# Kernel optimization log

Hardware: AMD Instinct MI355X
Metric: run time of the kernel (lower is better)

## Reference

```python
import jax, jax.numpy as jnp
import numpy as np

CHAMFER_WEIGHT = 1.0
REG_WEIGHT = 0.1


def setup_inputs() -> dict:
    key = jax.random.key(0)
    k1, k2, k3 = jax.random.split(key, 3)
    B, N, M, K = 16, 4096, 4096, 64
    return {
        "predicted_points": jax.random.normal(k1, (B, N, 3), dtype=jnp.float32),
        "ground_truth_points": jax.random.normal(k2, (B, M, 3), dtype=jnp.float32),
        "trans_feat": jax.random.normal(k3, (B, K, K), dtype=jnp.float32),
    }


def _chamfer(pred, target):
    # Euclidean (non-squared) pairwise distances, matching torch.cdist.
    # Gram trick avoids materializing [B,N,M,3].
    p2 = jnp.sum(pred * pred, axis=-1)          # [B,N]
    t2 = jnp.sum(target * target, axis=-1)      # [B,M]
    cross = jnp.einsum("bnd,bmd->bnm", pred, target)  # [B,N,M]
    d2 = p2[:, :, None] + t2[:, None, :] - 2.0 * cross
    dist = jnp.sqrt(jnp.maximum(d2, 0.0))       # [B,N,M]
    min1 = jnp.min(dist, axis=2)                # [B,N] pred -> nearest target
    min2 = jnp.min(dist, axis=1)                # [B,M] target -> nearest pred
    return jnp.mean(jnp.mean(min1, axis=1) + jnp.mean(min2, axis=1))


def _feature_transform_reg(trans):
    K = trans.shape[1]
    I = jnp.eye(K, dtype=trans.dtype)
    gram = jnp.einsum("bik,bjk->bij", trans, trans)  # trans @ trans^T
    # Frobenius norm per batch element, then mean over batch
    return jnp.mean(jnp.sqrt(jnp.sum((gram - I) ** 2, axis=(1, 2))))


def reference(predicted_points, ground_truth_points, trans_feat):
    chamfer = _chamfer(predicted_points, ground_truth_points)
    reg = _feature_transform_reg(trans_feat)
    return CHAMFER_WEIGHT * chamfer + REG_WEIGHT * reg
```

## Files before the change

### kernel.cpp

```cpp
#include <hip/hip_runtime.h>
#include <math.h>

#define BB 16
#define NN 4096
#define MM 4096
#define CHUNK_COLS 2048
#define NCHUNK (MM / CHUNK_COLS)

typedef __attribute__((ext_vector_type(8))) short bf16x8;
typedef __attribute__((ext_vector_type(16))) float f32x16;

static __device__ inline unsigned short f2bf(float f) {
    unsigned int u = __float_as_uint(f);
    return (unsigned short)((u + 0x7FFFu + ((u >> 16) & 1u)) >> 16);
}
static __device__ inline bf16x8 bzero() {
    bf16x8 z;
    #pragma unroll
    for (int i = 0; i < 8; ++i) z[i] = 0;
    return z;
}
static __device__ inline f32x16 fzero() {
    f32x16 z;
    #pragma unroll
    for (int i = 0; i < 16; ++i) z[i] = 0.f;
    return z;
}

__global__ __launch_bounds__(256, 4) void chamfer_kernel(
    const float* __restrict__ pred, const float* __restrict__ gt,
    float* __restrict__ out)
{
    __shared__ __align__(16) float smem[8832];
    __shared__ float ssum[4];

    const int tid  = threadIdx.x;
    const int lane = tid & 63;
    const int w    = tid >> 6;
    const int li   = lane & 31;
    const int hi   = lane >> 5;
    const int b    = blockIdx.y;
    const int dir  = blockIdx.z;
    const float* rows = dir ? gt : pred;
    const float* cols = dir ? pred : gt;
    const float* rb = rows + (size_t)b * NN * 3;
    const float* cb = cols + (size_t)b * MM * 3;

    const int r0 = blockIdx.x * 256 + w * 64;
    bf16x8 A0 = bzero(), A1 = bzero();
    if (lane < 32) {
        #pragma unroll
        for (int f = 0; f < 2; ++f) {
            const float* rp = rb + (size_t)(r0 + f * 32 + li) * 3;
            const float px = rp[0], py = rp[1], pz = rp[2];
            const float p2 = px * px + py * py + pz * pz;
            bf16x8 fr = bzero();
            fr[0] = (short)f2bf(-2.f * px);
            fr[1] = (short)f2bf(-2.f * py);
            fr[2] = (short)f2bf(-2.f * pz);
            fr[3] = (short)f2bf(p2);
            fr[4] = (short)0x3F80;
            if (f == 0) A0 = fr; else A1 = fr;
        }
    }

    float mv0[16], mv1[16];
    #pragma unroll
    for (int r = 0; r < 16; ++r) { mv0[r] = 3.4e38f; mv1[r] = 3.4e38f; }

    uint4* sB = (uint4*)smem;
    const bf16x8* sBf = (const bf16x8*)smem;

    for (int ch = 0; ch < NCHUNK; ++ch) {
        __syncthreads();
        #pragma unroll
        for (int i = 0; i < CHUNK_COLS / 256; ++i) {
            const int c = i * 256 + tid;
            const float* tp = cb + (size_t)(ch * CHUNK_COLS + c) * 3;
            const float tx = tp[0], ty = tp[1], tz = tp[2];
            const float t2 = tx * tx + ty * ty + tz * tz;
            uint4 pk;
            pk.x = (unsigned)f2bf(tx) | ((unsigned)f2bf(ty) << 16);
            pk.y = (unsigned)f2bf(tz) | (0x3F80u << 16);
            pk.z = (unsigned)f2bf(t2);
            pk.w = 0u;
            sB[c] = pk;
        }
        __syncthreads();

        #pragma unroll 2
        for (int jt = 0; jt < CHUNK_COLS / 64; ++jt) {
            bf16x8 b1 = bzero(), b2 = bzero();
            if (lane < 32) {
                b1 = sBf[jt * 64 + li];
                b2 = sBf[jt * 64 + 32 + li];
            }
            f32x16 a11 = __builtin_amdgcn_mfma_f32_32x32x16_bf16(A0, b1, fzero(), 0, 0, 0);
            f32x16 a12 = __builtin_amdgcn_mfma_f32_32x32x16_bf16(A0, b2, fzero(), 0, 0, 0);
            #pragma unroll
            for (int r = 0; r < 16; ++r)
                mv0[r] = fminf(fminf(a11[r], a12[r]), mv0[r]);
            f32x16 a21 = __builtin_amdgcn_mfma_f32_32x32x16_bf16(A1, b1, fzero(), 0, 0, 0);
            f32x16 a22 = __builtin_amdgcn_mfma_f32_32x32x16_bf16(A1, b2, fzero(), 0, 0, 0);
            #pragma unroll
            for (int r = 0; r < 16; ++r)
                mv1[r] = fminf(fminf(a21[r], a22[r]), mv1[r]);
        }
    }

    __syncthreads();
    {
        float* wb = smem + w * 2208 + li * 68;
        #pragma unroll
        for (int q = 0; q < 4; ++q) {
            const int rl = q * 8 + hi * 4;
            *(float4*)&wb[rl]      = make_float4(mv0[4*q], mv0[4*q+1], mv0[4*q+2], mv0[4*q+3]);
            *(float4*)&wb[rl + 32] = make_float4(mv1[4*q], mv1[4*q+1], mv1[4*q+2], mv1[4*q+3]);
        }
    }
    __syncthreads();

    const float* rbm = smem + (tid >> 6) * 2208 + (tid & 63);
    float m = 3.4e38f;
    #pragma unroll
    for (int c = 0; c < 32; ++c) m = fminf(m, rbm[c * 68]);
    float d = sqrtf(fmaxf(m, 0.0f));

    #pragma unroll
    for (int off = 32; off > 0; off >>= 1)
        d += __shfl_down(d, off, 64);
    if (lane == 0) ssum[w] = d;
    __syncthreads();
    if (tid == 0) {
        const float s = ssum[0] + ssum[1] + ssum[2] + ssum[3];
        atomicAdd(out, s * (1.0f / ((float)BB * (float)NN)));
    }
}

__global__ __launch_bounds__(64) void reg_kernel(
    const float* __restrict__ trans, float* __restrict__ out)
{
    const int b = blockIdx.x;
    const int lane = threadIdx.x;
    const int hi = lane >> 5, li = lane & 31;
    const float* T = trans + (size_t)b * 64 * 64;

    bf16x8 frag[2][4];
    #pragma unroll
    for (int h = 0; h < 2; ++h) {
        #pragma unroll
        for (int s = 0; s < 4; ++s) {
            const float* rp = T + (size_t)(h * 32 + li) * 64 + s * 16 + hi * 8;
            const float4 u0 = *(const float4*)rp;
            const float4 u1 = *(const float4*)(rp + 4);
            bf16x8 fr;
            fr[0] = (short)f2bf(u0.x); fr[1] = (short)f2bf(u0.y);
            fr[2] = (short)f2bf(u0.z); fr[3] = (short)f2bf(u0.w);
            fr[4] = (short)f2bf(u1.x); fr[5] = (short)f2bf(u1.y);
            fr[6] = (short)f2bf(u1.z); fr[7] = (short)f2bf(u1.w);
            frag[h][s] = fr;
        }
    }

    float fsum = 0.f;
    #pragma unroll
    for (int fi = 0; fi < 2; ++fi) {
        #pragma unroll
        for (int fj = 0; fj < 2; ++fj) {
            f32x16 a = fzero();
            #pragma unroll
            for (int s = 0; s < 4; ++s)
                a = __builtin_amdgcn_mfma_f32_32x32x16_bf16(frag[fi][s], frag[fj][s], a, 0, 0, 0);
            #pragma unroll
            for (int r = 0; r < 16; ++r) {
                const int row = fi * 32 + (r & 3) + 8 * (r >> 2) + 4 * hi;
                const int col = fj * 32 + li;
                const float d = a[r] - ((row == col) ? 1.0f : 0.0f);
                fsum = fmaf(d, d, fsum);
            }
        }
    }

    #pragma unroll
    for (int off = 32; off > 0; off >>= 1)
        fsum += __shfl_down(fsum, off, 64);
    if (lane == 0)
        atomicAdd(out, (0.1f / (float)BB) * sqrtf(fsum));
}

extern "C" void kernel_launch(void* const* d_in, const int* in_sizes, int n_in,
                              void* d_out, int out_size, void* d_ws, size_t ws_size,
                              hipStream_t stream)
{
    const float* pred  = (const float*)d_in[0];
    const float* gt    = (const float*)d_in[1];
    const float* trans = (const float*)d_in[2];
    float* out = (float*)d_out;

    hipMemsetAsync(out, 0, sizeof(float), stream);
    reg_kernel<<<dim3(BB), dim3(64), 0, stream>>>(trans, out);
    chamfer_kernel<<<dim3(NN / 256, BB, 2), dim3(256), 0, stream>>>(pred, gt, out);
}
```

Baseline: 32.80 us.

## Split column range across blocks with atomicMin merge and a separate finish kernel

Each chamfer block now covers only half of the column points, which doubles the grid so more blocks run per CU. Partial row minima are merged through an order-preserving unsigned atomicMin into a workspace buffer, and a new finish kernel takes the sqrt and the mean. The inner loop also prefetches the next LDS B fragments into registers, and the chunk loop with its repeated barriers is gone. The cost is a workspace memset, global atomics and one extra kernel launch.

Result: slower. 39.03 us (+19.0%).

```diff
diff --git a/kernel.cpp b/kernel.cpp
--- a/kernel.cpp
+++ b/kernel.cpp
@@ -4,8 +4,9 @@
 #define BB 16
 #define NN 4096
 #define MM 4096
-#define CHUNK_COLS 2048
-#define NCHUNK (MM / CHUNK_COLS)
+#define NSLICE 2
+#define SLICE_COLS (MM / NSLICE)
+#define NROWS_TOTAL (2 * BB * NN)
 
 typedef __attribute__((ext_vector_type(8))) short bf16x8;
 typedef __attribute__((ext_vector_type(16))) float f32x16;
@@ -27,26 +28,27 @@
     return z;
 }
 
-__global__ __launch_bounds__(256, 4) void chamfer_kernel(
+__global__ __launch_bounds__(256, 4) void chamfer_min_kernel(
     const float* __restrict__ pred, const float* __restrict__ gt,
-    float* __restrict__ out)
+    unsigned int* __restrict__ wsmin)
 {
     __shared__ __align__(16) float smem[8832];
-    __shared__ float ssum[4];
 
     const int tid  = threadIdx.x;
     const int lane = tid & 63;
     const int w    = tid >> 6;
     const int li   = lane & 31;
     const int hi   = lane >> 5;
+    const int tile   = blockIdx.x >> 1;
+    const int mslice = blockIdx.x & (NSLICE - 1);
     const int b    = blockIdx.y;
     const int dir  = blockIdx.z;
     const float* rows = dir ? gt : pred;
     const float* cols = dir ? pred : gt;
     const float* rb = rows + (size_t)b * NN * 3;
-    const float* cb = cols + (size_t)b * MM * 3;
-
-    const int r0 = blockIdx.x * 256 + w * 64;
+    const float* cb = cols + ((size_t)b * MM + (size_t)mslice * SLICE_COLS) * 3;
+
+    const int r0 = tile * 256 + w * 64;
     bf16x8 A0 = bzero(), A1 = bzero();
     if (lane < 32) {
         #pragma unroll
@@ -64,48 +66,45 @@
         }
     }
 
+    uint4* sB = (uint4*)smem;
+    #pragma unroll
+    for (int i = 0; i < SLICE_COLS / 256; ++i) {
+        const int c = i * 256 + tid;
+        const float* tp = cb + (size_t)c * 3;
+        const float tx = tp[0], ty = tp[1], tz = tp[2];
+        const float t2 = tx * tx + ty * ty + tz * tz;
+        uint4 pk;
+        pk.x = (unsigned)f2bf(tx) | ((unsigned)f2bf(ty) << 16);
+        pk.y = (unsigned)f2bf(tz) | (0x3F80u << 16);
+        pk.z = (unsigned)f2bf(t2);
+        pk.w = 0u;
+        sB[c] = pk;
+    }
+    __syncthreads();
+
     float mv0[16], mv1[16];
     #pragma unroll
     for (int r = 0; r < 16; ++r) { mv0[r] = 3.4e38f; mv1[r] = 3.4e38f; }
 
-    uint4* sB = (uint4*)smem;
     const bf16x8* sBf = (const bf16x8*)smem;
 
-    for (int ch = 0; ch < NCHUNK; ++ch) {
-        __syncthreads();
-        #pragma unroll
-        for (int i = 0; i < CHUNK_COLS / 256; ++i) {
-            const int c = i * 256 + tid;
-            const float* tp = cb + (size_t)(ch * CHUNK_COLS + c) * 3;
-            const float tx = tp[0], ty = tp[1], tz = tp[2];
-            const float t2 = tx * tx + ty * ty + tz * tz;
-            uint4 pk;
-            pk.x = (unsigned)f2bf(tx) | ((unsigned)f2bf(ty) << 16);
-            pk.y = (unsigned)f2bf(tz) | (0x3F80u << 16);
-            pk.z = (unsigned)f2bf(t2);
-            pk.w = 0u;
-            sB[c] = pk;
-        }
-        __syncthreads();
-
-        #pragma unroll 2
-        for (int jt = 0; jt < CHUNK_COLS / 64; ++jt) {
-            bf16x8 b1 = bzero(), b2 = bzero();
-            if (lane < 32) {
-                b1 = sBf[jt * 64 + li];
-                b2 = sBf[jt * 64 + 32 + li];
-            }
-            f32x16 a11 = __builtin_amdgcn_mfma_f32_32x32x16_bf16(A0, b1, fzero(), 0, 0, 0);
-            f32x16 a12 = __builtin_amdgcn_mfma_f32_32x32x16_bf16(A0, b2, fzero(), 0, 0, 0);
-            #pragma unroll
-            for (int r = 0; r < 16; ++r)
-                mv0[r] = fminf(fminf(a11[r], a12[r]), mv0[r]);
-            f32x16 a21 = __builtin_amdgcn_mfma_f32_32x32x16_bf16(A1, b1, fzero(), 0, 0, 0);
-            f32x16 a22 = __builtin_amdgcn_mfma_f32_32x32x16_bf16(A1, b2, fzero(), 0, 0, 0);
-            #pragma unroll
-            for (int r = 0; r < 16; ++r)
-                mv1[r] = fminf(fminf(a21[r], a22[r]), mv1[r]);
-        }
+    bf16x8 b1 = sBf[li], b2 = sBf[32 + li];
+    for (int jt = 0; jt < SLICE_COLS / 64; ++jt) {
+        const bf16x8 c1 = b1, c2 = b2;
+        if (jt + 1 < SLICE_COLS / 64) {
+            b1 = sBf[(jt + 1) * 64 + li];
+            b2 = sBf[(jt + 1) * 64 + 32 + li];
+        }
+        f32x16 a11 = __builtin_amdgcn_mfma_f32_32x32x16_bf16(A0, c1, fzero(), 0, 0, 0);
+        f32x16 a12 = __builtin_amdgcn_mfma_f32_32x32x16_bf16(A0, c2, fzero(), 0, 0, 0);
+        #pragma unroll
+        for (int r = 0; r < 16; ++r)
+            mv0[r] = fminf(fminf(a11[r], a12[r]), mv0[r]);
+        f32x16 a21 = __builtin_amdgcn_mfma_f32_32x32x16_bf16(A1, c1, fzero(), 0, 0, 0);
+        f32x16 a22 = __builtin_amdgcn_mfma_f32_32x32x16_bf16(A1, c2, fzero(), 0, 0, 0);
+        #pragma unroll
+        for (int r = 0; r < 16; ++r)
+            mv1[r] = fminf(fminf(a21[r], a22[r]), mv1[r]);
     }
 
     __syncthreads();
@@ -120,16 +119,31 @@
     }
     __syncthreads();
 
-    const float* rbm = smem + (tid >> 6) * 2208 + (tid & 63);
+    const float* rbm = smem + w * 2208 + lane;
     float m = 3.4e38f;
     #pragma unroll
     for (int c = 0; c < 32; ++c) m = fminf(m, rbm[c * 68]);
-    float d = sqrtf(fmaxf(m, 0.0f));
+
+    unsigned int u = __float_as_uint(m);
+    u = (u & 0x80000000u) ? ~u : (u | 0x80000000u);
+    const int rowg = (dir * BB + b) * NN + r0 + lane;
+    atomicMin(&wsmin[rowg], u);
+}
+
+__global__ __launch_bounds__(256) void chamfer_finish_kernel(
+    const unsigned int* __restrict__ wsmin, float* __restrict__ out)
+{
+    const int g = blockIdx.x * 256 + threadIdx.x;
+    unsigned int u = wsmin[g];
+    const unsigned int bts = (u & 0x80000000u) ? (u & 0x7fffffffu) : ~u;
+    float d = sqrtf(fmaxf(__uint_as_float(bts), 0.0f));
 
     #pragma unroll
     for (int off = 32; off > 0; off >>= 1)
         d += __shfl_down(d, off, 64);
-    if (lane == 0) ssum[w] = d;
+    __shared__ float ssum[4];
+    const int tid = threadIdx.x;
+    if ((tid & 63) == 0) ssum[tid >> 6] = d;
     __syncthreads();
     if (tid == 0) {
         const float s = ssum[0] + ssum[1] + ssum[2] + ssum[3];
@@ -196,8 +210,13 @@
     const float* gt    = (const float*)d_in[1];
     const float* trans = (const float*)d_in[2];
     float* out = (float*)d_out;
+    unsigned int* wsmin = (unsigned int*)d_ws;
 
     hipMemsetAsync(out, 0, sizeof(float), stream);
+    hipMemsetAsync(wsmin, 0xFF, (size_t)NROWS_TOTAL * sizeof(unsigned int), stream);
+
     reg_kernel<<<dim3(BB), dim3(64), 0, stream>>>(trans, out);
-    chamfer_kernel<<<dim3(NN / 256, BB, 2), dim3(256), 0, stream>>>(pred, gt, out);
-}
+    chamfer_min_kernel<<<dim3((NN / 256) * NSLICE, BB, 2), dim3(256), 0, stream>>>(
+        pred, gt, wsmin);
+    chamfer_finish_kernel<<<dim3(NROWS_TOTAL / 256), dim3(256), 0, stream>>>(wsmin, out);
+}
```
